# Kernel optimization log

Measured on AMD Instinct MI355X. Metric: run time of the kernel, lower is better.

The kernel has to match this reference:

```python
import jax, jax.numpy as jnp
import numpy as np

NODE_NUM = 100000
LAYER_NUM = 4
EMB = 128
FEAT = 256
BATCH = 4096
NEIGH = 32
EPS = 1e-12  # F.normalize default eps


def setup_inputs() -> dict:
    key = jax.random.key(0)
    ks = jax.random.split(key, 10)
    std = 1.0 / np.sqrt(EMB)
    return {
        "layers": jax.random.randint(ks[0], (BATCH,), 0, LAYER_NUM),
        "node_i": jax.random.randint(ks[1], (BATCH,), 0, NODE_NUM),
        "neighs_i": jax.random.randint(ks[2], (BATCH, LAYER_NUM, NEIGH), 0, NODE_NUM),
        "features": jax.random.normal(ks[3], (NODE_NUM, FEAT), dtype=jnp.float32),
        "layer_embs": jax.random.uniform(ks[4], (NODE_NUM, LAYER_NUM, EMB), dtype=jnp.float32, minval=-1.0, maxval=1.0),
        "neigh_emb_trans": jax.random.normal(ks[5], (LAYER_NUM, FEAT, EMB), dtype=jnp.float32) * std,
        "trans_weights": jax.random.normal(ks[6], (EMB, EMB), dtype=jnp.float32) * std,
        "trans_weights_s1": jax.random.normal(ks[7], (EMB, EMB), dtype=jnp.float32) * std,
        "trans_weights_s2": jax.random.normal(ks[8], (EMB, 1), dtype=jnp.float32) * std,
    }


def reference(layers, node_i, neighs_i, features, layer_embs, neigh_emb_trans,
              trans_weights, trans_weights_s1, trans_weights_s2):
    # Gather neighbor features: [B, L, J, F]
    feats_n = features[neighs_i]
    # Per-layer linear transform == diagonal of torch's 'bijk,akm->bijam' over (i,a):
    # [B, L, J, M]
    h = jnp.einsum('bljf,lfm->bljm', feats_n, neigh_emb_trans)
    # Sum over neighbors -> [B, L, M]
    h = h.sum(axis=2)
    # Attention over layers: tanh(h @ Ws1) @ Ws2 -> [B, L]
    scores = jnp.squeeze(jnp.tanh(h @ trans_weights_s1) @ trans_weights_s2, axis=-1)
    att = jax.nn.softmax(scores, axis=1)  # [B, L]
    # Attention-weighted layer aggregation -> [B, M]
    agg = jnp.einsum('bl,blm->bm', att, h)
    node_embed = agg @ trans_weights  # [B, M]
    final = node_embed + layer_embs[node_i, layers]  # residual with per-(node,layer) emb
    # F.normalize(dim=1): x / max(||x||_2, eps)
    norm = jnp.linalg.norm(final, axis=1, keepdims=True)
    return final / jnp.maximum(norm, EPS)
```

## Files before the change

### kernel.cpp

```cpp
#include <hip/hip_runtime.h>
#include <hip/hip_bf16.h>
#include <math.h>

#define BATCH 4096
#define LNUM  4
#define NEIGH 32
#define FEAT  256
#define EMB   128

#define B_TILE 4
#define ROWS   (B_TILE * LNUM)

__global__ __launch_bounds__(256, 4) void fused_liamne(
    const int* __restrict__ layers, const int* __restrict__ node_i,
    const int* __restrict__ neighs, const float* __restrict__ features,
    const float* __restrict__ layer_embs, const float* __restrict__ W,
    const float* __restrict__ Wt, const float* __restrict__ Ws1,
    const float* __restrict__ Ws2, float* __restrict__ out) {
  __shared__ float sS[ROWS][FEAT];
  __shared__ float sH[ROWS][EMB];
  __shared__ float sc[ROWS];

  int b0 = blockIdx.x * B_TILE;
  int tid = threadIdx.x;
  int w = tid >> 6;
  int lane = tid & 63;

  {
    int nIdx[LNUM];
#pragma unroll
    for (int l = 0; l < LNUM; ++l) {
      const int* nbr = neighs + ((size_t)(b0 + w) * LNUM + l) * NEIGH;
      nIdx[l] = nbr[lane & 31];
    }
    const float4* f4 = (const float4*)features;
    float4 acc[LNUM];
#pragma unroll
    for (int l = 0; l < LNUM; ++l) acc[l] = make_float4(0.f, 0.f, 0.f, 0.f);
#pragma unroll
    for (int jj = 0; jj < 8; ++jj) {
      float4 v[LNUM][4];
#pragma unroll
      for (int l = 0; l < LNUM; ++l)
#pragma unroll
        for (int q = 0; q < 4; ++q) {
          int n = __shfl(nIdx[l], jj * 4 + q, 64);
          v[l][q] = f4[(size_t)n * (FEAT / 4) + lane];
        }
#pragma unroll
      for (int l = 0; l < LNUM; ++l)
#pragma unroll
        for (int q = 0; q < 4; ++q) {
          acc[l].x += v[l][q].x; acc[l].y += v[l][q].y;
          acc[l].z += v[l][q].z; acc[l].w += v[l][q].w;
        }
    }
#pragma unroll
    for (int l = 0; l < LNUM; ++l)
      ((float4*)sS[w * LNUM + l])[lane] = acc[l];
  }
  __syncthreads();

  {
    const float* Wl = W + (size_t)w * FEAT * EMB;
    float acc[B_TILE][2] = {};
    for (int k = 0; k < FEAT; k += 4) {
      float4 s[B_TILE];
#pragma unroll
      for (int lb = 0; lb < B_TILE; ++lb)
        s[lb] = *(const float4*)&sS[lb * LNUM + w][k];
#pragma unroll
      for (int kk = 0; kk < 4; ++kk) {
        float2 wv = *(const float2*)&Wl[(size_t)(k + kk) * EMB + lane * 2];
#pragma unroll
        for (int lb = 0; lb < B_TILE; ++lb) {
          float sv = ((const float*)&s[lb])[kk];
          acc[lb][0] += sv * wv.x;
          acc[lb][1] += sv * wv.y;
        }
      }
    }
#pragma unroll
    for (int lb = 0; lb < B_TILE; ++lb)
      *(float2*)&sH[lb * LNUM + w][lane * 2] =
          make_float2(acc[lb][0], acc[lb][1]);
  }
  __syncthreads();

  {
    float acc[4][2] = {};
    for (int k = 0; k < EMB; k += 4) {
      float4 h[4];
#pragma unroll
      for (int i = 0; i < 4; ++i)
        h[i] = *(const float4*)&sH[w * 4 + i][k];
#pragma unroll
      for (int kk = 0; kk < 4; ++kk) {
        float2 wv = *(const float2*)&Ws1[(size_t)(k + kk) * EMB + lane * 2];
#pragma unroll
        for (int i = 0; i < 4; ++i) {
          float hv = ((const float*)&h[i])[kk];
          acc[i][0] += hv * wv.x;
          acc[i][1] += hv * wv.y;
        }
      }
    }
    float2 w2 = *(const float2*)&Ws2[lane * 2];
#pragma unroll
    for (int i = 0; i < 4; ++i) {
      float p = tanhf(acc[i][0]) * w2.x + tanhf(acc[i][1]) * w2.y;
#pragma unroll
      for (int m = 1; m < 64; m <<= 1) p += __shfl_xor(p, m, 64);
      if (lane == 0) sc[w * 4 + i] = p;
    }
  }
  __syncthreads();

  float* sAgg = &sS[0][0];
  for (int i = tid; i < B_TILE * EMB; i += 256) {
    int lb = i >> 7, m = i & 127;
    float s0 = sc[lb * 4 + 0], s1 = sc[lb * 4 + 1];
    float s2 = sc[lb * 4 + 2], s3 = sc[lb * 4 + 3];
    float mx = fmaxf(fmaxf(s0, s1), fmaxf(s2, s3));
    float e0 = expf(s0 - mx), e1 = expf(s1 - mx);
    float e2 = expf(s2 - mx), e3 = expf(s3 - mx);
    float inv = 1.0f / (e0 + e1 + e2 + e3);
    float a = e0 * sH[lb * 4 + 0][m] + e1 * sH[lb * 4 + 1][m] +
              e2 * sH[lb * 4 + 2][m] + e3 * sH[lb * 4 + 3][m];
    sAgg[i] = a * inv;
  }
  __syncthreads();

  {
    float ax = 0.f, ay = 0.f;
    for (int k = 0; k < EMB; ++k) {
      float2 wv = *(const float2*)&Wt[(size_t)k * EMB + lane * 2];
      float a = sAgg[w * EMB + k];
      ax += a * wv.x;
      ay += a * wv.y;
    }
    int b = b0 + w;
    int node = node_i[b];
    int lay = layers[b];
    float2 e = *(const float2*)&layer_embs[((size_t)node * LNUM + lay) * EMB +
                                           lane * 2];
    ax += e.x;
    ay += e.y;
    float ss = ax * ax + ay * ay;
#pragma unroll
    for (int m = 1; m < 64; m <<= 1) ss += __shfl_xor(ss, m, 64);
    float inv = 1.0f / fmaxf(sqrtf(ss), 1e-12f);
    *(float2*)&out[(size_t)b * EMB + lane * 2] =
        make_float2(ax * inv, ay * inv);
  }
}

extern "C" void kernel_launch(void* const* d_in, const int* in_sizes, int n_in,
                              void* d_out, int out_size, void* d_ws,
                              size_t ws_size, hipStream_t stream) {
  const int* layers = (const int*)d_in[0];
  const int* node_i = (const int*)d_in[1];
  const int* neighs = (const int*)d_in[2];
  const float* features = (const float*)d_in[3];
  const float* layer_embs = (const float*)d_in[4];
  const float* neigh_emb_trans = (const float*)d_in[5];
  const float* trans_weights = (const float*)d_in[6];
  const float* trans_weights_s1 = (const float*)d_in[7];
  const float* trans_weights_s2 = (const float*)d_in[8];
  float* out = (float*)d_out;

  fused_liamne<<<dim3(BATCH / B_TILE), 256, 0, stream>>>(
      layers, node_i, neighs, features, layer_embs, neigh_emb_trans,
      trans_weights, trans_weights_s1, trans_weights_s2, out);
}
```

Before: 397.9 us.

## Split into bf16 feature conversion, tiled gather-GEMM, and attention kernels

```diff
diff --git a/kernel.cpp b/kernel.cpp
--- a/kernel.cpp
+++ b/kernel.cpp
@@ -1,5 +1,4 @@
 #include <hip/hip_runtime.h>
-#include <hip/hip_bf16.h>
 #include <math.h>
 
 #define BATCH 4096
@@ -7,117 +6,168 @@
 #define NEIGH 32
 #define FEAT  256
 #define EMB   128
-
-#define B_TILE 4
-#define ROWS   (B_TILE * LNUM)
-
-__global__ __launch_bounds__(256, 4) void fused_liamne(
-    const int* __restrict__ layers, const int* __restrict__ node_i,
-    const int* __restrict__ neighs, const float* __restrict__ features,
-    const float* __restrict__ layer_embs, const float* __restrict__ W,
-    const float* __restrict__ Wt, const float* __restrict__ Ws1,
-    const float* __restrict__ Ws2, float* __restrict__ out) {
-  __shared__ float sS[ROWS][FEAT];
-  __shared__ float sH[ROWS][EMB];
-  __shared__ float sc[ROWS];
-
-  int b0 = blockIdx.x * B_TILE;
+#define NODES 100000
+
+__device__ __forceinline__ unsigned int f2bf(float x) {
+  unsigned int u = __float_as_uint(x);
+  return (u + 0x7fffu + ((u >> 16) & 1u)) >> 16;
+}
+
+__global__ __launch_bounds__(256) void k_convert(
+    const float* __restrict__ f, unsigned short* __restrict__ fb) {
+  size_t i0 = ((size_t)blockIdx.x * 256 + threadIdx.x) * 8;
+  float4 a = *(const float4*)(f + i0);
+  float4 b = *(const float4*)(f + i0 + 4);
+  uint4 o;
+  o.x = f2bf(a.x) | (f2bf(a.y) << 16);
+  o.y = f2bf(a.z) | (f2bf(a.w) << 16);
+  o.z = f2bf(b.x) | (f2bf(b.y) << 16);
+  o.w = f2bf(b.z) | (f2bf(b.w) << 16);
+  *(uint4*)(fb + i0) = o;
+}
+
+__global__ __launch_bounds__(256, 2) void k12(
+    const int* __restrict__ neighs, const unsigned short* __restrict__ fb,
+    const float* __restrict__ W, float* __restrict__ H) {
+  __shared__ float sS[32][260];
+  __shared__ float sW[32][128];
+  int b0 = blockIdx.x * 32;
+  int l = blockIdx.y;
   int tid = threadIdx.x;
-  int w = tid >> 6;
-  int lane = tid & 63;
+  int w = tid >> 6, lane = tid & 63;
+
+  int nIdx[8];
+#pragma unroll
+  for (int i = 0; i < 8; ++i) {
+    const int* nbr = neighs + ((size_t)(b0 + w * 8 + i) * LNUM + l) * NEIGH;
+    nIdx[i] = nbr[lane & 31];
+  }
+  const uint2* f2 = (const uint2*)fb;
+#pragma unroll
+  for (int i = 0; i < 8; i += 2) {
+    float acc0[4] = {0.f, 0.f, 0.f, 0.f};
+    float acc1[4] = {0.f, 0.f, 0.f, 0.f};
+#pragma unroll
+    for (int jj = 0; jj < 8; ++jj) {
+      uint2 va[4], vb[4];
+#pragma unroll
+      for (int q = 0; q < 4; ++q) {
+        int na = __shfl(nIdx[i], jj * 4 + q, 64);
+        va[q] = f2[(size_t)na * 64 + lane];
+      }
+#pragma unroll
+      for (int q = 0; q < 4; ++q) {
+        int nb = __shfl(nIdx[i + 1], jj * 4 + q, 64);
+        vb[q] = f2[(size_t)nb * 64 + lane];
+      }
+#pragma unroll
+      for (int q = 0; q < 4; ++q) {
+        acc0[0] += __uint_as_float(va[q].x << 16);
+        acc0[1] += __uint_as_float(va[q].x & 0xffff0000u);
+        acc0[2] += __uint_as_float(va[q].y << 16);
+        acc0[3] += __uint_as_float(va[q].y & 0xffff0000u);
+        acc1[0] += __uint_as_float(vb[q].x << 16);
+        acc1[1] += __uint_as_float(vb[q].x & 0xffff0000u);
+        acc1[2] += __uint_as_float(vb[q].y << 16);
+        acc1[3] += __uint_as_float(vb[q].y & 0xffff0000u);
+      }
+    }
+    *(float4*)&sS[w * 8 + i][lane * 4] =
+        make_float4(acc0[0], acc0[1], acc0[2], acc0[3]);
+    *(float4*)&sS[w * 8 + i + 1][lane * 4] =
+        make_float4(acc1[0], acc1[1], acc1[2], acc1[3]);
+  }
+  __syncthreads();
+
+  int tx = tid & 31;
+  int ty = tid >> 5;
+  float acc[4][4] = {};
+  const float* Wl = W + (size_t)l * FEAT * EMB;
+  for (int k0 = 0; k0 < FEAT; k0 += 32) {
+#pragma unroll
+    for (int t = 0; t < 4; ++t) {
+      int idx = tid + t * 256;
+      int kk = idx >> 5;
+      int cc = idx & 31;
+      *(float4*)&sW[kk][cc * 4] =
+          *(const float4*)&Wl[(size_t)(k0 + kk) * EMB + cc * 4];
+    }
+    __syncthreads();
+#pragma unroll
+    for (int kc = 0; kc < 32; kc += 4) {
+      float4 s4[4];
+#pragma unroll
+      for (int r = 0; r < 4; ++r)
+        s4[r] = *(const float4*)&sS[ty * 4 + r][k0 + kc];
+#pragma unroll
+      for (int kk = 0; kk < 4; ++kk) {
+        float4 wv = *(const float4*)&sW[kc + kk][tx * 4];
+#pragma unroll
+        for (int r = 0; r < 4; ++r) {
+          float sv = ((const float*)&s4[r])[kk];
+          acc[r][0] += sv * wv.x; acc[r][1] += sv * wv.y;
+          acc[r][2] += sv * wv.z; acc[r][3] += sv * wv.w;
+        }
+      }
+    }
+    __syncthreads();
+  }
+#pragma unroll
+  for (int r = 0; r < 4; ++r) {
+    int b = b0 + ty * 4 + r;
+    *(float4*)&H[((size_t)b * LNUM + l) * EMB + tx * 4] =
+        make_float4(acc[r][0], acc[r][1], acc[r][2], acc[r][3]);
+  }
+}
+
+__global__ __launch_bounds__(256, 2) void k34(
+    const float* __restrict__ H, const float* __restrict__ Ws1,
+    const float* __restrict__ Ws2, const float* __restrict__ Wt,
+    const int* __restrict__ node_i, const int* __restrict__ layers,
+    const float* __restrict__ layer_embs, float* __restrict__ out) {
+  __shared__ float sHH[64][130];
+  __shared__ float sAgg[16][128];
+  __shared__ float sc[64];
+  int b0 = blockIdx.x * 16;
+  int tid = threadIdx.x;
+  int w = tid >> 6, lane = tid & 63;
 
   {
-    int nIdx[LNUM];
-#pragma unroll
-    for (int l = 0; l < LNUM; ++l) {
-      const int* nbr = neighs + ((size_t)(b0 + w) * LNUM + l) * NEIGH;
-      nIdx[l] = nbr[lane & 31];
-    }
-    const float4* f4 = (const float4*)features;
-    float4 acc[LNUM];
-#pragma unroll
-    for (int l = 0; l < LNUM; ++l) acc[l] = make_float4(0.f, 0.f, 0.f, 0.f);
-#pragma unroll
-    for (int jj = 0; jj < 8; ++jj) {
-      float4 v[LNUM][4];
-#pragma unroll
-      for (int l = 0; l < LNUM; ++l)
-#pragma unroll
-        for (int q = 0; q < 4; ++q) {
-          int n = __shfl(nIdx[l], jj * 4 + q, 64);
-          v[l][q] = f4[(size_t)n * (FEAT / 4) + lane];
-        }
-#pragma unroll
-      for (int l = 0; l < LNUM; ++l)
-#pragma unroll
-        for (int q = 0; q < 4; ++q) {
-          acc[l].x += v[l][q].x; acc[l].y += v[l][q].y;
-          acc[l].z += v[l][q].z; acc[l].w += v[l][q].w;
-        }
-    }
-#pragma unroll
-    for (int l = 0; l < LNUM; ++l)
-      ((float4*)sS[w * LNUM + l])[lane] = acc[l];
+    const float4* Hp = (const float4*)(H + (size_t)b0 * LNUM * EMB);
+    for (int i = tid; i < 64 * 32; i += 256) {
+      int r = i >> 5, c = i & 31;
+      *(float4*)&sHH[r][c * 4] = Hp[i];
+    }
   }
   __syncthreads();
 
   {
-    const float* Wl = W + (size_t)w * FEAT * EMB;
-    float acc[B_TILE][2] = {};
-    for (int k = 0; k < FEAT; k += 4) {
-      float4 s[B_TILE];
-#pragma unroll
-      for (int lb = 0; lb < B_TILE; ++lb)
-        s[lb] = *(const float4*)&sS[lb * LNUM + w][k];
-#pragma unroll
-      for (int kk = 0; kk < 4; ++kk) {
-        float2 wv = *(const float2*)&Wl[(size_t)(k + kk) * EMB + lane * 2];
-#pragma unroll
-        for (int lb = 0; lb < B_TILE; ++lb) {
-          float sv = ((const float*)&s[lb])[kk];
-          acc[lb][0] += sv * wv.x;
-          acc[lb][1] += sv * wv.y;
-        }
-      }
-    }
-#pragma unroll
-    for (int lb = 0; lb < B_TILE; ++lb)
-      *(float2*)&sH[lb * LNUM + w][lane * 2] =
-          make_float2(acc[lb][0], acc[lb][1]);
-  }
-  __syncthreads();
-
-  {
-    float acc[4][2] = {};
-    for (int k = 0; k < EMB; k += 4) {
-      float4 h[4];
-#pragma unroll
-      for (int i = 0; i < 4; ++i)
-        h[i] = *(const float4*)&sH[w * 4 + i][k];
-#pragma unroll
-      for (int kk = 0; kk < 4; ++kk) {
-        float2 wv = *(const float2*)&Ws1[(size_t)(k + kk) * EMB + lane * 2];
-#pragma unroll
-        for (int i = 0; i < 4; ++i) {
-          float hv = ((const float*)&h[i])[kk];
-          acc[i][0] += hv * wv.x;
-          acc[i][1] += hv * wv.y;
-        }
-      }
-    }
-    float2 w2 = *(const float2*)&Ws2[lane * 2];
-#pragma unroll
-    for (int i = 0; i < 4; ++i) {
-      float p = tanhf(acc[i][0]) * w2.x + tanhf(acc[i][1]) * w2.y;
+    float acc[16][2] = {};
+    for (int k = 0; k < EMB; k += 2) {
+      float2 h2[16];
+#pragma unroll
+      for (int r = 0; r < 16; ++r)
+        h2[r] = *(const float2*)&sHH[w * 16 + r][k];
+      float2 w0 = *(const float2*)&Ws1[(size_t)k * EMB + lane * 2];
+      float2 w1 = *(const float2*)&Ws1[(size_t)(k + 1) * EMB + lane * 2];
+#pragma unroll
+      for (int r = 0; r < 16; ++r) {
+        acc[r][0] += h2[r].x * w0.x + h2[r].y * w1.x;
+        acc[r][1] += h2[r].x * w0.y + h2[r].y * w1.y;
+      }
+    }
+    float2 w2v = *(const float2*)&Ws2[lane * 2];
+#pragma unroll
+    for (int r = 0; r < 16; ++r) {
+      float p = tanhf(acc[r][0]) * w2v.x + tanhf(acc[r][1]) * w2v.y;
 #pragma unroll
       for (int m = 1; m < 64; m <<= 1) p += __shfl_xor(p, m, 64);
-      if (lane == 0) sc[w * 4 + i] = p;
-    }
-  }
-  __syncthreads();
-
-  float* sAgg = &sS[0][0];
-  for (int i = tid; i < B_TILE * EMB; i += 256) {
+      if (lane == 0) sc[w * 16 + r] = p;
+    }
+  }
+  __syncthreads();
+
+  for (int i = tid; i < 16 * EMB; i += 256) {
     int lb = i >> 7, m = i & 127;
     float s0 = sc[lb * 4 + 0], s1 = sc[lb * 4 + 1];
     float s2 = sc[lb * 4 + 2], s3 = sc[lb * 4 + 3];
@@ -125,33 +175,38 @@
     float e0 = expf(s0 - mx), e1 = expf(s1 - mx);
     float e2 = expf(s2 - mx), e3 = expf(s3 - mx);
     float inv = 1.0f / (e0 + e1 + e2 + e3);
-    float a = e0 * sH[lb * 4 + 0][m] + e1 * sH[lb * 4 + 1][m] +
-              e2 * sH[lb * 4 + 2][m] + e3 * sH[lb * 4 + 3][m];
-    sAgg[i] = a * inv;
+    float a = e0 * sHH[lb * 4 + 0][m] + e1 * sHH[lb * 4 + 1][m] +
+              e2 * sHH[lb * 4 + 2][m] + e3 * sHH[lb * 4 + 3][m];
+    sAgg[lb][m] = a * inv;
   }
   __syncthreads();
 
   {
-    float ax = 0.f, ay = 0.f;
+    float ax[4] = {0.f, 0.f, 0.f, 0.f}, ay[4] = {0.f, 0.f, 0.f, 0.f};
     for (int k = 0; k < EMB; ++k) {
       float2 wv = *(const float2*)&Wt[(size_t)k * EMB + lane * 2];
-      float a = sAgg[w * EMB + k];
-      ax += a * wv.x;
-      ay += a * wv.y;
-    }
-    int b = b0 + w;
-    int node = node_i[b];
-    int lay = layers[b];
-    float2 e = *(const float2*)&layer_embs[((size_t)node * LNUM + lay) * EMB +
-                                           lane * 2];
-    ax += e.x;
-    ay += e.y;
-    float ss = ax * ax + ay * ay;
-#pragma unroll
-    for (int m = 1; m < 64; m <<= 1) ss += __shfl_xor(ss, m, 64);
-    float inv = 1.0f / fmaxf(sqrtf(ss), 1e-12f);
-    *(float2*)&out[(size_t)b * EMB + lane * 2] =
-        make_float2(ax * inv, ay * inv);
+#pragma unroll
+      for (int g = 0; g < 4; ++g) {
+        float a = sAgg[w * 4 + g][k];
+        ax[g] += a * wv.x;
+        ay[g] += a * wv.y;
+      }
+    }
+#pragma unroll
+    for (int g = 0; g < 4; ++g) {
+      int b = b0 + w * 4 + g;
+      int node = node_i[b];
+      int lay = layers[b];
+      float2 e = *(const float2*)&layer_embs[((size_t)node * LNUM + lay) * EMB +
+                                             lane * 2];
+      float vx = ax[g] + e.x, vy = ay[g] + e.y;
+      float ss = vx * vx + vy * vy;
+#pragma unroll
+      for (int m = 1; m < 64; m <<= 1) ss += __shfl_xor(ss, m, 64);
+      float inv = 1.0f / fmaxf(sqrtf(ss), 1e-12f);
+      *(float2*)&out[(size_t)b * EMB + lane * 2] =
+          make_float2(vx * inv, vy * inv);
+    }
   }
 }
 
@@ -169,7 +224,12 @@
   const float* trans_weights_s2 = (const float*)d_in[8];
   float* out = (float*)d_out;
 
-  fused_liamne<<<dim3(BATCH / B_TILE), 256, 0, stream>>>(
-      layers, node_i, neighs, features, layer_embs, neigh_emb_trans,
-      trans_weights, trans_weights_s1, trans_weights_s2, out);
-}
+  unsigned short* fb = (unsigned short*)d_ws;
+  float* H = (float*)((char*)d_ws + (size_t)NODES * FEAT * sizeof(unsigned short));
+
+  k_convert<<<dim3(NODES * FEAT / (256 * 8)), 256, 0, stream>>>(features, fb);
+  k12<<<dim3(BATCH / 32, LNUM), 256, 0, stream>>>(neighs, fb, neigh_emb_trans, H);
+  k34<<<dim3(BATCH / 16), 256, 0, stream>>>(H, trans_weights_s1,
+                                            trans_weights_s2, trans_weights,
+                                            node_i, layers, layer_embs, out);
+}
```

New measurement: 415.3 us. +4.4%, slower.
